# Kernel optimization log

Hardware: AMD Instinct MI355X
Metric: run time of the kernel (lower is better)

## Reference

```python
import jax, jax.numpy as jnp
import numpy as np

WX, WY = 32, 32
N = WX * WY                      # 1024 tokens
TOKEN_DIM = 1024
QKV = 512
H = 8
HD = QKV // H                    # 64
TOPK = 32
B = 64
NUM_UNIQUE = (2 * WX - 1) * (2 * WY - 1)  # 3969 unique relative offsets
LN_EPS = 1e-5


def _make_rel_idx():
    # identical to torch create_positional_biases: lexicographic unique index of (dx, dy)
    ix = np.arange(N) // WY
    iy = np.arange(N) % WY
    dx = ix[:, None] - ix[None, :]
    dy = iy[:, None] - iy[None, :]
    rel = (dx + WX - 1) * (2 * WY - 1) + (dy + WY - 1)
    return jnp.asarray(rel, dtype=jnp.int32)  # [N, N]


def _layernorm(x, g, b):
    m = jnp.mean(x, axis=-1, keepdims=True)
    v = jnp.mean(jnp.square(x - m), axis=-1, keepdims=True)
    return (x - m) * jax.lax.rsqrt(v + LN_EPS) * g + b


def setup_inputs() -> dict:
    key = jax.random.key(0)
    ks = jax.random.split(key, 12)
    s = 0.02
    return {
        "x": jax.random.normal(ks[0], (B, N, TOKEN_DIM), jnp.float32),
        "scorer_w": jax.random.normal(ks[1], (1, TOKEN_DIM), jnp.float32) * s,
        "scorer_b": jnp.zeros((1,), jnp.float32),
        "ln_g": jnp.ones((TOKEN_DIM,), jnp.float32),
        "ln_b": jnp.zeros((TOKEN_DIM,), jnp.float32),
        "qk_w": jax.random.normal(ks[2], (QKV, TOKEN_DIM), jnp.float32) * s,
        "qk_b": jnp.zeros((QKV,), jnp.float32),
        "v_w": jax.random.normal(ks[3], (QKV, TOKEN_DIM), jnp.float32) * s,
        "v_b": jnp.zeros((QKV,), jnp.float32),
        "skip_w": jax.random.normal(ks[4], (QKV, TOKEN_DIM), jnp.float32) * s,
        "skip_b": jnp.zeros((QKV,), jnp.float32),
        "out_w": jax.random.normal(ks[5], (QKV, QKV), jnp.float32) * s,
        "out_b": jnp.zeros((QKV,), jnp.float32),
        "fc_w": jax.random.normal(ks[6], (2, QKV), jnp.float32) * s,
        "fc_b": jnp.zeros((2,), jnp.float32),
        "unique_bias": jax.random.normal(ks[7], (NUM_UNIQUE,), jnp.float32) * s,
        "rel_idx": _make_rel_idx(),
    }


def reference(x, scorer_w, scorer_b, ln_g, ln_b, qk_w, qk_b, v_w, v_b,
              skip_w, skip_b, out_w, out_b, fc_w, fc_b, unique_bias, rel_idx):
    # token selection (eval path: argmax of relevance logits)
    logits = jnp.einsum('bnd,od->bno', x, scorer_w)[..., 0] + scorer_b[0]  # [B, N]
    sel_idx = jnp.argmax(logits, axis=-1)                                   # [B]
    sel_tok = x[jnp.arange(B), sel_idx]                                     # [B, D]

    x_n = _layernorm(x, ln_g, ln_b)
    s_n = _layernorm(sel_tok, ln_g, ln_b)

    value = (jnp.einsum('bnd,qd->bnq', x_n, v_w) + v_b).reshape(B, N, H, HD).transpose(0, 2, 1, 3)  # [B,H,N,hd]
    key_t = (jnp.einsum('bnd,qd->bnq', x_n, qk_w) + qk_b).reshape(B, N, H, HD).transpose(0, 2, 1, 3)
    query = (s_n @ qk_w.T + qk_b).reshape(B, H, HD)                         # [B,H,hd]

    attn = jnp.einsum('bhd,bhnd->bhn', query, key_t) / jnp.sqrt(jnp.float32(HD))  # [B,H,N]
    bias = unique_bias[rel_idx[sel_idx]]                                    # gather: [B, N]
    attn = jax.nn.softmax(attn + bias[:, None, :], axis=-1)

    # top-k sparsification + renormalization
    _, topk_idx = jax.lax.top_k(attn, TOPK)                                 # [B,H,K]
    mask = jax.nn.one_hot(topk_idx, N, dtype=attn.dtype).sum(axis=-2)       # [B,H,N] 0/1
    attn = attn * mask
    attn = attn / (attn.sum(axis=-1, keepdims=True) + 1e-9)

    y = jnp.einsum('bhn,bhnd->bhd', attn, value).reshape(B, QKV)            # [B, QKV]
    skip = sel_tok @ skip_w.T + skip_b
    y = jax.nn.relu(y + skip)
    # dropout is identity in eval mode
    y = y @ out_w.T + out_b
    y = y @ fc_w.T + fc_b
    return y  # [B, 2]
```

## Files before the change

### kernel.cpp

```cpp
#include <hip/hip_runtime.h>
#include <hip/hip_bf16.h>
#include <math.h>

#define WX 32
#define WY 32
#define NTOK 1024
#define TD 1024
#define QKV 512
#define NH 8
#define HD 64
#define TOPK 32
#define BB 64

__device__ __forceinline__ float wred_sum(float v){
  #pragma unroll
  for (int o=32;o;o>>=1) v += __shfl_xor(v,o,64);
  return v;
}
__device__ __forceinline__ float wred_max(float v){
  #pragma unroll
  for (int o=32;o;o>>=1) v = fmaxf(v, __shfl_xor(v,o,64));
  return v;
}
__device__ __forceinline__ float dot4f(float4 a, float4 b){
  return a.x*b.x + a.y*b.y + a.z*b.z + a.w*b.w;
}

__global__ __launch_bounds__(256) void k1_stats(
    const float* __restrict__ x, const float* __restrict__ sw, const float* __restrict__ sb,
    float* __restrict__ mean, float* __restrict__ rstd, float* __restrict__ logit){
  int wave = threadIdx.x >> 6, lane = threadIdx.x & 63;
  int tok = blockIdx.x*4 + wave;
  const float4* xp = (const float4*)(x + (size_t)tok*TD);
  const float4* sp = (const float4*)sw;
  float s1=0.f, s2=0.f, sd=0.f;
  #pragma unroll
  for (int j=0;j<4;j++){
    float4 v = xp[lane + j*64];
    float4 w = sp[lane + j*64];
    s1 += v.x+v.y+v.z+v.w;
    s2 += v.x*v.x + v.y*v.y + v.z*v.z + v.w*v.w;
    sd += dot4f(v,w);
  }
  s1 = wred_sum(s1); s2 = wred_sum(s2); sd = wred_sum(sd);
  if (lane==0){
    float m = s1*(1.f/1024.f);
    float var = s2*(1.f/1024.f) - m*m;
    mean[tok] = m;
    rstd[tok] = rsqrtf(var + 1e-5f);
    logit[tok] = sd + sb[0];
  }
}

__global__ __launch_bounds__(256) void k2_prep(
    const float* __restrict__ x, const float* __restrict__ logit,
    const float* __restrict__ mean, const float* __restrict__ rstd,
    const float* __restrict__ lng, const float* __restrict__ lnb,
    const float* __restrict__ qkw, const float* __restrict__ qkb,
    const int* __restrict__ relIdx, const float* __restrict__ ub,
    int* __restrict__ selI, float* __restrict__ gu8,
    float* __restrict__ Aw, float* __restrict__ C0w, float* __restrict__ biasArr){
  __shared__ float sn[TD];
  __shared__ float qs[HD];
  __shared__ float red[256];
  __shared__ float redV[4]; __shared__ int redI[4];
  __shared__ int sel_s;
  int b = blockIdx.x >> 3, h = blockIdx.x & 7;
  int t = threadIdx.x, lane = t&63, wave = t>>6;

  const float* lg = logit + b*NTOK;
  float bv = -INFINITY; int bi = 0;
  #pragma unroll
  for (int j=0;j<4;j++){ int idx = t*4+j; float v = lg[idx]; if (v > bv){ bv=v; bi=idx; } }
  #pragma unroll
  for (int o=32;o;o>>=1){
    float vv = __shfl_xor(bv,o,64); int ii = __shfl_xor(bi,o,64);
    if (vv > bv || (vv == bv && ii < bi)){ bv=vv; bi=ii; }
  }
  if (lane==0){ redV[wave]=bv; redI[wave]=bi; }
  __syncthreads();
  if (t==0){
    float v = redV[0]; int i = redI[0];
    for (int w=1; w<4; w++){ if (redV[w] > v || (redV[w]==v && redI[w]<i)){ v=redV[w]; i=redI[w]; } }
    sel_s = i;
    if (h==0) selI[b] = i;
  }
  __syncthreads();
  int sel = sel_s;
  float m = mean[b*NTOK+sel], r = rstd[b*NTOK+sel];
  float4 g4 = ((const float4*)lng)[t];
  float4 b4 = ((const float4*)lnb)[t];
  {
    float4 xv = ((const float4*)(x + ((size_t)b*NTOK + sel)*TD))[t];
    float4 s4;
    s4.x = (xv.x-m)*r*g4.x + b4.x;
    s4.y = (xv.y-m)*r*g4.y + b4.y;
    s4.z = (xv.z-m)*r*g4.z + b4.z;
    s4.w = (xv.w-m)*r*g4.w + b4.w;
    ((float4*)sn)[t] = s4;
  }
  __syncthreads();
  {
    int row = t>>2, part = t&3;
    const float4* wr = (const float4*)(qkw + (size_t)(h*HD+row)*TD + part*256);
    const float4* xp = ((const float4*)sn) + part*64;
    float acc = 0.f;
    #pragma unroll 8
    for (int j=0;j<64;j++) acc += dot4f(wr[j], xp[j]);
    red[t] = acc;
  }
  __syncthreads();
  if (t < HD) qs[t] = red[t*4]+red[t*4+1]+red[t*4+2]+red[t*4+3] + qkb[h*HD+t];
  __syncthreads();
  float4 acc = make_float4(0.f,0.f,0.f,0.f);
  for (int c=0;c<HD;c++){
    float qv = qs[c];
    float4 w = ((const float4*)(qkw + (size_t)(h*HD+c)*TD))[t];
    acc.x += qv*w.x; acc.y += qv*w.y; acc.z += qv*w.z; acc.w += qv*w.w;
  }
  {
    float4 gu;
    gu.x = acc.x*g4.x*0.125f; gu.y = acc.y*g4.y*0.125f;
    gu.z = acc.z*g4.z*0.125f; gu.w = acc.w*g4.w*0.125f;
    ((float4*)(gu8 + ((size_t)(b*NH+h))*TD))[t] = gu;
  }
  float su_p = g4.x*acc.x + g4.y*acc.y + g4.z*acc.z + g4.w*acc.w;
  float bu_p = b4.x*acc.x + b4.y*acc.y + b4.z*acc.z + b4.w*acc.w;
  su_p = wred_sum(su_p); bu_p = wred_sum(bu_p);
  if (lane==0){ red[wave] = su_p; red[8+wave] = bu_p; }
  if (wave==0){
    float qb_p = qs[lane]*qkb[h*HD+lane];
    qb_p = wred_sum(qb_p);
    if (lane==0) red[16] = qb_p;
  }
  __syncthreads();
  if (t==0){
    float s  = red[0]+red[1]+red[2]+red[3];
    float bb = red[8]+red[9]+red[10]+red[11];
    Aw[b*NH+h]  = s*0.125f;
    C0w[b*NH+h] = (bb + red[16])*0.125f;
  }
  if (h==0){
    const int* rp = relIdx + (size_t)sel*NTOK;
    #pragma unroll
    for (int j=0;j<4;j++){
      int n = t*4+j;
      biasArr[b*NTOK+n] = ub[rp[n]];
    }
  }
}

__global__ __launch_bounds__(256) void k3_attn(
    const float* __restrict__ x, const float* __restrict__ mean, const float* __restrict__ rstd,
    const float* __restrict__ gu8, const float* __restrict__ Aw, const float* __restrict__ C0w,
    const float* __restrict__ biasArr, float* __restrict__ attL){
  int b = blockIdx.x >> 4;
  int chunk = blockIdx.x & 15;
  int lane = threadIdx.x & 63, wave = threadIdx.x >> 6;

  const float4* gp = (const float4*)(gu8 + (size_t)b*NH*TD);
  float4 G[NH][4];
  #pragma unroll
  for (int h=0;h<NH;h++)
    #pragma unroll
    for (int j=0;j<4;j++)
      G[h][j] = gp[h*256 + j*64 + lane];
  float Ah[NH], Ch[NH];
  #pragma unroll
  for (int h=0;h<NH;h++){ Ah[h] = Aw[b*NH+h]; Ch[h] = C0w[b*NH+h]; }

  const int base = chunk*64 + wave*16;
  float4 cur[4];
  {
    const float4* xp = (const float4*)(x + ((size_t)b*NTOK + base)*TD);
    #pragma unroll
    for (int j=0;j<4;j++) cur[j] = xp[j*64 + lane];
  }
  for (int i=0;i<16;i++){
    int n = base + i;
    int tok = b*NTOK + n;
    float4 nxt[4];
    if (i < 15){
      const float4* xp = (const float4*)(x + (size_t)(tok+1)*TD);
      #pragma unroll
      for (int j=0;j<4;j++) nxt[j] = xp[j*64 + lane];
    }
    float m = mean[tok], r = rstd[tok], bias = biasArr[b*NTOK+n];
    float s[NH];
    #pragma unroll
    for (int h=0;h<NH;h++){
      float a = dot4f(cur[0],G[h][0]) + dot4f(cur[1],G[h][1])
              + dot4f(cur[2],G[h][2]) + dot4f(cur[3],G[h][3]);
      s[h] = wred_sum(a);
    }
    #pragma unroll
    for (int h=0;h<NH;h++){
      if (lane == h)
        attL[((size_t)b*NH+h)*NTOK + n] = r*s[h] - r*m*Ah[h] + Ch[h] + bias;
    }
    if (i < 15){
      #pragma unroll
      for (int j=0;j<4;j++) cur[j] = nxt[j];
    }
  }
}

__global__ __launch_bounds__(256) void k4_topkv(
    const float* __restrict__ x, const float* __restrict__ mean, const float* __restrict__ rstd,
    const float* __restrict__ lng, const float* __restrict__ lnb,
    const float* __restrict__ vw, const float* __restrict__ vb,
    const float* __restrict__ attL, float* __restrict__ yout){
  __shared__ float redf[4];
  __shared__ float wtopV[4][TOPK]; __shared__ int wtopI[4][TOPK];
  __shared__ float selV[TOPK]; __shared__ int selIs[TOPK];
  __shared__ float Ssh;
  __shared__ float aa[TOPK]; __shared__ float am[TOPK];
  __shared__ float xbar[TD];
  __shared__ float red2[256];
  int b = blockIdx.x >> 3, h = blockIdx.x & 7;
  int t = threadIdx.x, lane = t&63, wave = t>>6;

  float4 Lv = ((const float4*)(attL + ((size_t)b*NH + h)*NTOK))[t];
  float lm = fmaxf(fmaxf(Lv.x,Lv.y), fmaxf(Lv.z,Lv.w));
  lm = wred_max(lm);
  if (lane==0) redf[wave] = lm;
  __syncthreads();
  float maxL = fmaxf(fmaxf(redf[0],redf[1]), fmaxf(redf[2],redf[3]));
  __syncthreads();
  float ev[4];
  ev[0] = __expf(Lv.x - maxL); ev[1] = __expf(Lv.y - maxL);
  ev[2] = __expf(Lv.z - maxL); ev[3] = __expf(Lv.w - maxL);
  float zp = ev[0]+ev[1]+ev[2]+ev[3];
  zp = wred_sum(zp);
  if (lane==0) redf[wave] = zp;
  __syncthreads();
  float Z = redf[0]+redf[1]+redf[2]+redf[3];

  for (int k=0;k<TOPK;k++){
    float bv = -1.f; int bi = 1<<20;
    #pragma unroll
    for (int j=0;j<4;j++){ if (ev[j] > bv){ bv = ev[j]; bi = t*4+j; } }
    #pragma unroll
    for (int o=32;o;o>>=1){
      float vv = __shfl_xor(bv,o,64); int ii = __shfl_xor(bi,o,64);
      if (vv > bv || (vv == bv && ii < bi)){ bv=vv; bi=ii; }
    }
    #pragma unroll
    for (int j=0;j<4;j++){ if (bi == t*4+j) ev[j] = -1.f; }
    if (lane==0){ wtopV[wave][k] = bv; wtopI[wave][k] = bi; }
  }
  __syncthreads();
  if (t==0){
    int p0=0,p1=0,p2=0,p3=0;
    float S = 0.f;
    for (int k=0;k<TOPK;k++){
      float bv = -1.f; int bi = 1<<20, bw = 0;
      float v; int ii;
      v = wtopV[0][p0]; ii = wtopI[0][p0]; if (v > bv || (v==bv && ii<bi)){ bv=v; bi=ii; bw=0; }
      v = wtopV[1][p1]; ii = wtopI[1][p1]; if (v > bv || (v==bv && ii<bi)){ bv=v; bi=ii; bw=1; }
      v = wtopV[2][p2]; ii = wtopI[2][p2]; if (v > bv || (v==bv && ii<bi)){ bv=v; bi=ii; bw=2; }
      v = wtopV[3][p3]; ii = wtopI[3][p3]; if (v > bv || (v==bv && ii<bi)){ bv=v; bi=ii; bw=3; }
      if (bw==0) p0 = (p0<TOPK-1)?p0+1:p0;
      else if (bw==1) p1 = (p1<TOPK-1)?p1+1:p1;
      else if (bw==2) p2 = (p2<TOPK-1)?p2+1:p2;
      else p3 = (p3<TOPK-1)?p3+1:p3;
      selV[k] = bv; selIs[k] = bi; S += bv;
    }
    Ssh = S;
  }
  __syncthreads();
  float S = Ssh;
  float denom = S + 1e-9f*Z;
  float W = S/denom;
  if (t < TOPK){
    int ni = selIs[t];
    float w = selV[t]/denom;
    float a = w * rstd[b*NTOK+ni];
    aa[t] = a; am[t] = a*mean[b*NTOK+ni];
  }
  __syncthreads();
  float c = 0.f;
  #pragma unroll
  for (int k=0;k<TOPK;k++) c += am[k];

  float4 acc = make_float4(0.f,0.f,0.f,0.f);
  for (int k=0;k<TOPK;k++){
    float a = aa[k];
    float4 xv = ((const float4*)(x + ((size_t)b*NTOK + selIs[k])*TD))[t];
    acc.x += a*xv.x; acc.y += a*xv.y; acc.z += a*xv.z; acc.w += a*xv.w;
  }
  float4 g4 = ((const float4*)lng)[t];
  float4 b4 = ((const float4*)lnb)[t];
  float4 xb;
  xb.x = g4.x*(acc.x - c) + b4.x*W;
  xb.y = g4.y*(acc.y - c) + b4.y*W;
  xb.z = g4.z*(acc.z - c) + b4.z*W;
  xb.w = g4.w*(acc.w - c) + b4.w*W;
  ((float4*)xbar)[t] = xb;
  __syncthreads();

  int co = t >> 2, part = t & 3;
  const float4* vp = (const float4*)(vw + (size_t)(h*HD+co)*TD + part*256);
  const float4* xp2 = ((const float4*)xbar) + part*64;
  float a2 = 0.f;
  #pragma unroll 8
  for (int j=0;j<64;j++) a2 += dot4f(vp[j], xp2[j]);
  red2[t] = a2;
  __syncthreads();
  if (part==0){
    float y = red2[t] + red2[t+1] + red2[t+2] + red2[t+3] + vb[h*HD+co]*W;
    yout[b*QKV + h*HD + co] = y;
  }
}

__global__ __launch_bounds__(256) void k5a(
    const float* __restrict__ x, const int* __restrict__ selI,
    const float* __restrict__ skw, const float* __restrict__ skb,
    const float* __restrict__ yv, float* __restrict__ t1ws){
  __shared__ float xs[TD];
  __shared__ float red[256];
  int b = blockIdx.x >> 3, chunk = blockIdx.x & 7;
  int t = threadIdx.x;
  int sel = selI[b];
  ((float4*)xs)[t] = ((const float4*)(x + ((size_t)b*NTOK + sel)*TD))[t];
  __syncthreads();
  int row = chunk*64 + (t>>2), part = t&3;
  const float4* wr = (const float4*)(skw + (size_t)row*TD + part*256);
  const float4* xp = ((const float4*)xs) + part*64;
  float acc = 0.f;
  #pragma unroll 8
  for (int j=0;j<64;j++) acc += dot4f(wr[j], xp[j]);
  red[t] = acc;
  __syncthreads();
  if (part==0){
    float v = red[t]+red[t+1]+red[t+2]+red[t+3];
    t1ws[b*QKV+row] = fmaxf(yv[b*QKV+row] + v + skb[row], 0.f);
  }
}

__global__ __launch_bounds__(256) void k5b(
    const float* __restrict__ t1ws, const float* __restrict__ ow,
    const float* __restrict__ ob, float* __restrict__ t2ws){
  __shared__ float ts[QKV];
  __shared__ float red[256];
  int b = blockIdx.x >> 3, chunk = blockIdx.x & 7;
  int t = threadIdx.x;
  if (t < 128) ((float4*)ts)[t] = ((const float4*)(t1ws + (size_t)b*QKV))[t];
  __syncthreads();
  int row = chunk*64 + (t>>2), part = t&3;
  const float4* wr = (const float4*)(ow + (size_t)row*QKV + part*128);
  const float4* xp = ((const float4*)ts) + part*32;
  float acc = 0.f;
  #pragma unroll
  for (int j=0;j<32;j++) acc += dot4f(wr[j], xp[j]);
  red[t] = acc;
  __syncthreads();
  if (part==0)
    t2ws[b*QKV+row] = red[t]+red[t+1]+red[t+2]+red[t+3] + ob[row];
}

__global__ __launch_bounds__(64) void k5c(
    const float* __restrict__ t2ws, const float* __restrict__ fcw,
    const float* __restrict__ fcb, float* __restrict__ out){
  int b = blockIdx.x, lane = threadIdx.x;
  float a0 = 0.f, a1 = 0.f;
  #pragma unroll
  for (int j=0;j<8;j++){
    int d = j*64 + lane;
    float v = t2ws[(size_t)b*QKV + d];
    a0 += v*fcw[d]; a1 += v*fcw[QKV+d];
  }
  a0 = wred_sum(a0); a1 = wred_sum(a1);
  if (lane==0){ out[b*2+0] = a0 + fcb[0]; out[b*2+1] = a1 + fcb[1]; }
}

extern "C" void kernel_launch(void* const* d_in, const int* in_sizes, int n_in,
                              void* d_out, int out_size, void* d_ws, size_t ws_size,
                              hipStream_t stream) {
  const float* x   = (const float*)d_in[0];
  const float* sw  = (const float*)d_in[1];
  const float* sb  = (const float*)d_in[2];
  const float* lng = (const float*)d_in[3];
  const float* lnb = (const float*)d_in[4];
  const float* qkw = (const float*)d_in[5];
  const float* qkb = (const float*)d_in[6];
  const float* vw  = (const float*)d_in[7];
  const float* vb  = (const float*)d_in[8];
  const float* skw = (const float*)d_in[9];
  const float* skb = (const float*)d_in[10];
  const float* ow  = (const float*)d_in[11];
  const float* ob  = (const float*)d_in[12];
  const float* fcw = (const float*)d_in[13];
  const float* fcb = (const float*)d_in[14];
  const float* ub  = (const float*)d_in[15];
  const int*   ri  = (const int*)d_in[16];
  float* out = (float*)d_out;

  float* wsf     = (float*)d_ws;
  float* logit   = wsf;
  float* mean    = wsf + 65536;
  float* rstd    = wsf + 131072;
  int*   selI    = (int*)(wsf + 196608);
  float* gu8     = wsf + 196672;
  float* Aw      = wsf + 720960;
  float* C0w     = wsf + 721472;
  float* biasArr = wsf + 721984;
  float* attL    = wsf + 787520;
  float* yv      = wsf + 1311808;
  float* t1ws    = wsf + 1344576;
  float* t2ws    = wsf + 1377344;

  k1_stats<<<16384, 256, 0, stream>>>(x, sw, sb, mean, rstd, logit);
  k2_prep<<<BB*NH, 256, 0, stream>>>(x, logit, mean, rstd, lng, lnb, qkw, qkb,
                                     ri, ub, selI, gu8, Aw, C0w, biasArr);
  k3_attn<<<BB*16, 256, 0, stream>>>(x, mean, rstd, gu8, Aw, C0w, biasArr, attL);
  k4_topkv<<<BB*NH, 256, 0, stream>>>(x, mean, rstd, lng, lnb, vw, vb, attL, yv);
  k5a<<<BB*8, 256, 0, stream>>>(x, selI, skw, skb, yv, t1ws);
  k5b<<<BB*8, 256, 0, stream>>>(t1ws, ow, ob, t2ws);
  k5c<<<BB, 64, 0, stream>>>(t2ws, fcw, fcb, out);
}
```

Before: 557.0 us.

## Pipeline row loads in stats, coalesce attention stores, parallelize top-k merge

The stats kernel now has each wave process four tokens, prefetching the next row while reducing the current one, and launches a quarter as many blocks. The attention-logit kernel stages its per-head results in shared memory and writes them out as coalesced rows instead of scattered single-lane stores. The top-k merge, previously a serial loop on one thread, becomes a parallel rank computation over the 128 per-wave candidates. Several GEMV inner loops split into two accumulators to shorten dependency chains, which slightly changes the floating-point summation order.

After: 547.1 us, median of 2. Within noise of the previous version (-1.8%).

```diff
diff --git a/kernel.cpp b/kernel.cpp
--- a/kernel.cpp
+++ b/kernel.cpp
@@ -30,25 +30,40 @@
     const float* __restrict__ x, const float* __restrict__ sw, const float* __restrict__ sb,
     float* __restrict__ mean, float* __restrict__ rstd, float* __restrict__ logit){
   int wave = threadIdx.x >> 6, lane = threadIdx.x & 63;
-  int tok = blockIdx.x*4 + wave;
-  const float4* xp = (const float4*)(x + (size_t)tok*TD);
+  int tok0 = blockIdx.x*16 + wave*4;
   const float4* sp = (const float4*)sw;
-  float s1=0.f, s2=0.f, sd=0.f;
-  #pragma unroll
-  for (int j=0;j<4;j++){
-    float4 v = xp[lane + j*64];
-    float4 w = sp[lane + j*64];
-    s1 += v.x+v.y+v.z+v.w;
-    s2 += v.x*v.x + v.y*v.y + v.z*v.z + v.w*v.w;
-    sd += dot4f(v,w);
-  }
-  s1 = wred_sum(s1); s2 = wred_sum(s2); sd = wred_sum(sd);
-  if (lane==0){
-    float m = s1*(1.f/1024.f);
-    float var = s2*(1.f/1024.f) - m*m;
-    mean[tok] = m;
-    rstd[tok] = rsqrtf(var + 1e-5f);
-    logit[tok] = sd + sb[0];
+  float4 w0 = sp[lane], w1 = sp[64+lane], w2 = sp[128+lane], w3 = sp[192+lane];
+  float sb0 = sb[0];
+  float4 cur[4];
+  {
+    const float4* xp = (const float4*)(x + (size_t)tok0*TD);
+    cur[0]=xp[lane]; cur[1]=xp[64+lane]; cur[2]=xp[128+lane]; cur[3]=xp[192+lane];
+  }
+  #pragma unroll
+  for (int i=0;i<4;i++){
+    int tok = tok0 + i;
+    float4 nxt[4];
+    if (i<3){
+      const float4* xp = (const float4*)(x + (size_t)(tok+1)*TD);
+      nxt[0]=xp[lane]; nxt[1]=xp[64+lane]; nxt[2]=xp[128+lane]; nxt[3]=xp[192+lane];
+    }
+    float s1=0.f, s2=0.f, sd=0.f;
+    s1 += cur[0].x+cur[0].y+cur[0].z+cur[0].w;  s2 += dot4f(cur[0],cur[0]);  sd += dot4f(cur[0],w0);
+    s1 += cur[1].x+cur[1].y+cur[1].z+cur[1].w;  s2 += dot4f(cur[1],cur[1]);  sd += dot4f(cur[1],w1);
+    s1 += cur[2].x+cur[2].y+cur[2].z+cur[2].w;  s2 += dot4f(cur[2],cur[2]);  sd += dot4f(cur[2],w2);
+    s1 += cur[3].x+cur[3].y+cur[3].z+cur[3].w;  s2 += dot4f(cur[3],cur[3]);  sd += dot4f(cur[3],w3);
+    s1 = wred_sum(s1); s2 = wred_sum(s2); sd = wred_sum(sd);
+    if (lane==0){
+      float m = s1*(1.f/1024.f);
+      float var = s2*(1.f/1024.f) - m*m;
+      mean[tok] = m;
+      rstd[tok] = rsqrtf(var + 1e-5f);
+      logit[tok] = sd + sb0;
+    }
+    if (i<3){
+      #pragma unroll
+      for (int j=0;j<4;j++) cur[j] = nxt[j];
+    }
   }
 }
 
@@ -104,20 +119,26 @@
     int row = t>>2, part = t&3;
     const float4* wr = (const float4*)(qkw + (size_t)(h*HD+row)*TD + part*256);
     const float4* xp = ((const float4*)sn) + part*64;
-    float acc = 0.f;
-    #pragma unroll 8
-    for (int j=0;j<64;j++) acc += dot4f(wr[j], xp[j]);
-    red[t] = acc;
+    float a0 = 0.f, a1 = 0.f;
+    #pragma unroll 4
+    for (int j=0;j<64;j+=2){ a0 += dot4f(wr[j], xp[j]); a1 += dot4f(wr[j+1], xp[j+1]); }
+    red[t] = a0 + a1;
   }
   __syncthreads();
   if (t < HD) qs[t] = red[t*4]+red[t*4+1]+red[t*4+2]+red[t*4+3] + qkb[h*HD+t];
   __syncthreads();
-  float4 acc = make_float4(0.f,0.f,0.f,0.f);
-  for (int c=0;c<HD;c++){
-    float qv = qs[c];
-    float4 w = ((const float4*)(qkw + (size_t)(h*HD+c)*TD))[t];
-    acc.x += qv*w.x; acc.y += qv*w.y; acc.z += qv*w.z; acc.w += qv*w.w;
-  }
+  float4 accE = make_float4(0.f,0.f,0.f,0.f);
+  float4 accO = make_float4(0.f,0.f,0.f,0.f);
+  #pragma unroll 4
+  for (int c=0;c<HD;c+=2){
+    float q0 = qs[c], q1 = qs[c+1];
+    float4 w0 = ((const float4*)(qkw + (size_t)(h*HD+c)*TD))[t];
+    float4 w1 = ((const float4*)(qkw + (size_t)(h*HD+c+1)*TD))[t];
+    accE.x += q0*w0.x; accE.y += q0*w0.y; accE.z += q0*w0.z; accE.w += q0*w0.w;
+    accO.x += q1*w1.x; accO.y += q1*w1.y; accO.z += q1*w1.z; accO.w += q1*w1.w;
+  }
+  float4 acc;
+  acc.x = accE.x+accO.x; acc.y = accE.y+accO.y; acc.z = accE.z+accO.z; acc.w = accE.w+accO.w;
   {
     float4 gu;
     gu.x = acc.x*g4.x*0.125f; gu.y = acc.y*g4.y*0.125f;
@@ -154,6 +175,7 @@
     const float* __restrict__ x, const float* __restrict__ mean, const float* __restrict__ rstd,
     const float* __restrict__ gu8, const float* __restrict__ Aw, const float* __restrict__ C0w,
     const float* __restrict__ biasArr, float* __restrict__ attL){
+  __shared__ float sL[NH*65];
   int b = blockIdx.x >> 4;
   int chunk = blockIdx.x & 15;
   int lane = threadIdx.x & 63, wave = threadIdx.x >> 6;
@@ -196,12 +218,18 @@
     #pragma unroll
     for (int h=0;h<NH;h++){
       if (lane == h)
-        attL[((size_t)b*NH+h)*NTOK + n] = r*s[h] - r*m*Ah[h] + Ch[h] + bias;
+        sL[h*65 + wave*16 + i] = r*s[h] - r*m*Ah[h] + Ch[h] + bias;
     }
     if (i < 15){
       #pragma unroll
       for (int j=0;j<4;j++) cur[j] = nxt[j];
     }
+  }
+  __syncthreads();
+  #pragma unroll
+  for (int hh=0; hh<2; hh++){
+    int h = wave + hh*4;
+    attL[((size_t)b*NH+h)*NTOK + chunk*64 + lane] = sL[h*65 + lane];
   }
 }
 
@@ -211,9 +239,8 @@
     const float* __restrict__ vw, const float* __restrict__ vb,
     const float* __restrict__ attL, float* __restrict__ yout){
   __shared__ float redf[4];
-  __shared__ float wtopV[4][TOPK]; __shared__ int wtopI[4][TOPK];
+  __shared__ float cV[128]; __shared__ int cI[128];
   __shared__ float selV[TOPK]; __shared__ int selIs[TOPK];
-  __shared__ float Ssh;
   __shared__ float aa[TOPK]; __shared__ float am[TOPK];
   __shared__ float xbar[TD];
   __shared__ float red2[256];
@@ -235,6 +262,7 @@
   if (lane==0) redf[wave] = zp;
   __syncthreads();
   float Z = redf[0]+redf[1]+redf[2]+redf[3];
+  __syncthreads();
 
   for (int k=0;k<TOPK;k++){
     float bv = -1.f; int bi = 1<<20;
@@ -247,29 +275,28 @@
     }
     #pragma unroll
     for (int j=0;j<4;j++){ if (bi == t*4+j) ev[j] = -1.f; }
-    if (lane==0){ wtopV[wave][k] = bv; wtopI[wave][k] = bi; }
-  }
-  __syncthreads();
-  if (t==0){
-    int p0=0,p1=0,p2=0,p3=0;
-    float S = 0.f;
-    for (int k=0;k<TOPK;k++){
-      float bv = -1.f; int bi = 1<<20, bw = 0;
-      float v; int ii;
-      v = wtopV[0][p0]; ii = wtopI[0][p0]; if (v > bv || (v==bv && ii<bi)){ bv=v; bi=ii; bw=0; }
-      v = wtopV[1][p1]; ii = wtopI[1][p1]; if (v > bv || (v==bv && ii<bi)){ bv=v; bi=ii; bw=1; }
-      v = wtopV[2][p2]; ii = wtopI[2][p2]; if (v > bv || (v==bv && ii<bi)){ bv=v; bi=ii; bw=2; }
-      v = wtopV[3][p3]; ii = wtopI[3][p3]; if (v > bv || (v==bv && ii<bi)){ bv=v; bi=ii; bw=3; }
-      if (bw==0) p0 = (p0<TOPK-1)?p0+1:p0;
-      else if (bw==1) p1 = (p1<TOPK-1)?p1+1:p1;
-      else if (bw==2) p2 = (p2<TOPK-1)?p2+1:p2;
-      else p3 = (p3<TOPK-1)?p3+1:p3;
-      selV[k] = bv; selIs[k] = bi; S += bv;
-    }
-    Ssh = S;
-  }
-  __syncthreads();
-  float S = Ssh;
+    if (lane==0){ cV[wave*TOPK+k] = bv; cI[wave*TOPK+k] = bi; }
+  }
+  __syncthreads();
+  float selContrib = 0.f;
+  if (t < 128){
+    float v = cV[t]; int idx = cI[t];
+    int rank = 0;
+    #pragma unroll 8
+    for (int j0=0;j0<32;j0++){
+      float4 v4 = ((float4*)cV)[j0];
+      int4  i4 = ((int4*)cI)[j0];
+      rank += (v4.x > v) || (v4.x==v && i4.x<idx);
+      rank += (v4.y > v) || (v4.y==v && i4.y<idx);
+      rank += (v4.z > v) || (v4.z==v && i4.z<idx);
+      rank += (v4.w > v) || (v4.w==v && i4.w<idx);
+    }
+    if (rank < TOPK){ selV[rank]=v; selIs[rank]=idx; selContrib = v; }
+  }
+  float Sp = wred_sum(selContrib);
+  if (lane==0) redf[wave] = Sp;
+  __syncthreads();
+  float S = redf[0]+redf[1]+redf[2]+redf[3];
   float denom = S + 1e-9f*Z;
   float W = S/denom;
   if (t < TOPK){
@@ -302,10 +329,10 @@
   int co = t >> 2, part = t & 3;
   const float4* vp = (const float4*)(vw + (size_t)(h*HD+co)*TD + part*256);
   const float4* xp2 = ((const float4*)xbar) + part*64;
-  float a2 = 0.f;
-  #pragma unroll 8
-  for (int j=0;j<64;j++) a2 += dot4f(vp[j], xp2[j]);
-  red2[t] = a2;
+  float a0 = 0.f, a1 = 0.f;
+  #pragma unroll 4
+  for (int j=0;j<64;j+=2){ a0 += dot4f(vp[j], xp2[j]); a1 += dot4f(vp[j+1], xp2[j+1]); }
+  red2[t] = a0 + a1;
   __syncthreads();
   if (part==0){
     float y = red2[t] + red2[t+1] + red2[t+2] + red2[t+3] + vb[h*HD+co]*W;
@@ -327,10 +354,10 @@
   int row = chunk*64 + (t>>2), part = t&3;
   const float4* wr = (const float4*)(skw + (size_t)row*TD + part*256);
   const float4* xp = ((const float4*)xs) + part*64;
-  float acc = 0.f;
-  #pragma unroll 8
-  for (int j=0;j<64;j++) acc += dot4f(wr[j], xp[j]);
-  red[t] = acc;
+  float a0 = 0.f, a1 = 0.f;
+  #pragma unroll 4
+  for (int j=0;j<64;j+=2){ a0 += dot4f(wr[j], xp[j]); a1 += dot4f(wr[j+1], xp[j+1]); }
+  red[t] = a0 + a1;
   __syncthreads();
   if (part==0){
     float v = red[t]+red[t+1]+red[t+2]+red[t+3];
@@ -410,7 +437,7 @@
   float* t1ws    = wsf + 1344576;
   float* t2ws    = wsf + 1377344;
 
-  k1_stats<<<16384, 256, 0, stream>>>(x, sw, sb, mean, rstd, logit);
+  k1_stats<<<4096, 256, 0, stream>>>(x, sw, sb, mean, rstd, logit);
   k2_prep<<<BB*NH, 256, 0, stream>>>(x, logit, mean, rstd, lng, lnb, qkw, qkb,
                                      ri, ub, selI, gu8, Aw, C0w, biasArr);
   k3_attn<<<BB*16, 256, 0, stream>>>(x, mean, rstd, gu8, Aw, C0w, biasArr, attL);
```
